# Optimization experiments

Measured on AMD Instinct MI355X. Metric: run time of the kernel, lower is better.

Reference implementation:

```python
import jax, jax.numpy as jnp
import numpy as np

EMB = 768
HEADS = 12
HEAD_DIM = EMB // HEADS
SEQ = 4096
BATCH = 1


def setup_inputs() -> dict:
    key = jax.random.key(0)
    ks = jax.random.split(key, 9)
    s = 1.0 / np.sqrt(EMB)
    return {
        "x": jax.random.normal(ks[0], (BATCH, SEQ, EMB), dtype=jnp.float32),
        "wq": jax.random.normal(ks[1], (EMB, EMB), dtype=jnp.float32) * s,
        "bq": jax.random.normal(ks[2], (EMB,), dtype=jnp.float32) * s,
        "wk": jax.random.normal(ks[3], (EMB, EMB), dtype=jnp.float32) * s,
        "bk": jax.random.normal(ks[4], (EMB,), dtype=jnp.float32) * s,
        "wv": jax.random.normal(ks[5], (EMB, EMB), dtype=jnp.float32) * s,
        "bv": jax.random.normal(ks[6], (EMB,), dtype=jnp.float32) * s,
        "wo": jax.random.normal(ks[7], (EMB, EMB), dtype=jnp.float32) * s,
        "bo": jax.random.normal(ks[8], (EMB,), dtype=jnp.float32) * s,
    }


def reference(x, wq, bq, wk, bk, wv, bv, wo, bo):
    b, n, _ = x.shape
    # projections: [b, n, emb] -> [b, heads, n, head_dim]
    def split_heads(t):
        return t.reshape(b, n, HEADS, HEAD_DIM).transpose(0, 2, 1, 3)
    q = split_heads(x @ wq + bq)
    k = split_heads(x @ wk + bk)
    v = split_heads(x @ wv + bv)
    # full N x N scores (naive attention, as in the original)
    scores = jnp.einsum("bhqd,bhkd->bhqk", q, k)
    causal = jnp.triu(jnp.ones((n, n), dtype=bool), k=1)
    scores = jnp.where(causal, -jnp.inf, scores)
    weights = jax.nn.softmax(scores / np.sqrt(HEAD_DIM), axis=-1)
    # dropout with rate 0.0 is identity (eval mode)
    ctx = jnp.einsum("bhqk,bhkd->bhqd", weights, v)
    ctx = ctx.transpose(0, 2, 1, 3).reshape(b, n, EMB)
    return ctx @ wo + bo
```

## Files before the change

kernel.cpp:

```cpp
#include <hip/hip_runtime.h>
#include <stdint.h>

#define SEQ 4096
#define EMB 768
#define HEADS 12
#define HD 64
#define NQT (SEQ / 64)

typedef __attribute__((ext_vector_type(8))) short short8;
typedef __attribute__((ext_vector_type(4))) short short4v;
typedef __attribute__((ext_vector_type(8))) __bf16 bf16x8;
typedef __attribute__((ext_vector_type(4))) __bf16 bf16x4;
typedef __attribute__((ext_vector_type(4))) float f32x4;

#define QSCALE 0.18033688011112043f

static __device__ __forceinline__ unsigned short f2bf(float f) {
    unsigned int u = __builtin_bit_cast(unsigned int, f);
    unsigned int r = 0x7fffu + ((u >> 16) & 1u);
    u += r;
    return (unsigned short)(u >> 16);
}

static __device__ __forceinline__ f32x4 mfma32(short8 a, short8 b, f32x4 c) {
    return __builtin_amdgcn_mfma_f32_16x16x32_bf16(
        __builtin_bit_cast(bf16x8, a), __builtin_bit_cast(bf16x8, b), c, 0, 0, 0);
}

static __device__ __forceinline__ f32x4 mfma16(short4v a, short4v b, f32x4 c) {
#if __has_builtin(__builtin_amdgcn_mfma_f32_16x16x16_bf16)
    return __builtin_amdgcn_mfma_f32_16x16x16_bf16(
        __builtin_bit_cast(bf16x4, a), __builtin_bit_cast(bf16x4, b), c, 0, 0, 0);
#else
    return __builtin_amdgcn_mfma_f32_16x16x16bf16_1k(a, b, c, 0, 0, 0);
#endif
}

static __device__ __forceinline__ short4v pack4bf(float a, float b, float c, float d) {
#if __has_builtin(__builtin_amdgcn_cvt_pk_bf16_f32)
    typedef __attribute__((ext_vector_type(2))) __bf16 bf16x2;
    bf16x2 lo = __builtin_amdgcn_cvt_pk_bf16_f32(a, b);
    bf16x2 hi = __builtin_amdgcn_cvt_pk_bf16_f32(c, d);
    uint2 u = {__builtin_bit_cast(unsigned int, lo), __builtin_bit_cast(unsigned int, hi)};
    return __builtin_bit_cast(short4v, u);
#else
    short4v p;
    p[0] = (short)f2bf(a); p[1] = (short)f2bf(b);
    p[2] = (short)f2bf(c); p[3] = (short)f2bf(d);
    return p;
#endif
}

static __device__ __forceinline__ void load_lds16(const void* g, void* l) {
    __builtin_amdgcn_global_load_lds(
        (const __attribute__((address_space(1))) unsigned int*)(uintptr_t)g,
        (__attribute__((address_space(3))) unsigned int*)(uintptr_t)l, 16, 0, 0);
}

__global__ __launch_bounds__(256) void convert_x(const float* __restrict__ x,
                                                 unsigned short* __restrict__ xb) {
    int i = blockIdx.x * 256 + threadIdx.x;
    float4 v = ((const float4*)x)[i];
    ushort4 o = {f2bf(v.x), f2bf(v.y), f2bf(v.z), f2bf(v.w)};
    ((ushort4*)xb)[i] = o;
}

__global__ __launch_bounds__(256) void convert_w(const float* __restrict__ wq,
                                                 const float* __restrict__ wk,
                                                 const float* __restrict__ wv,
                                                 const float* __restrict__ wo,
                                                 unsigned short* __restrict__ wqkvT,
                                                 unsigned short* __restrict__ woT) {
    __shared__ unsigned short Ls[64][72];
    const int z = blockIdx.z;
    const float* W = (z == 0) ? wq : (z == 1) ? wk : (z == 2) ? wv : wo;
    unsigned short* dst = (z < 3) ? (wqkvT + (size_t)z * EMB * EMB) : woT;
    const int k0 = blockIdx.x * 64, n0 = blockIdx.y * 64;
    const int r = threadIdx.x >> 2, c0 = (threadIdx.x & 3) * 16;
    for (int j = 0; j < 16; j += 4) {
        float4 v = *(const float4*)&W[(size_t)(k0 + r) * EMB + n0 + c0 + j];
        Ls[r][c0 + j] = f2bf(v.x);
        Ls[r][c0 + j + 1] = f2bf(v.y);
        Ls[r][c0 + j + 2] = f2bf(v.z);
        Ls[r][c0 + j + 3] = f2bf(v.w);
    }
    __syncthreads();
    unsigned short tmp[16];
    for (int j = 0; j < 16; j++) tmp[j] = Ls[c0 + j][r];
    *(uint4*)&dst[(size_t)(n0 + r) * EMB + k0 + c0] = *(uint4*)tmp;
    *(uint4*)&dst[(size_t)(n0 + r) * EMB + k0 + c0 + 8] = *(uint4*)(tmp + 8);
}

template <int MODE>
__global__ __launch_bounds__(256) void gemm128(const unsigned short* __restrict__ A,
                                               const unsigned short* __restrict__ Bt,
                                               const float* __restrict__ b0p,
                                               const float* __restrict__ b1p,
                                               const float* __restrict__ b2p,
                                               unsigned short* __restrict__ Qb,
                                               unsigned short* __restrict__ Kb,
                                               unsigned short* __restrict__ Vtb,
                                               float* __restrict__ outp) {
    __shared__ __align__(16) unsigned short As[128 * 32];
    __shared__ __align__(16) unsigned short Bs[128 * 32];
    const int tid = threadIdx.x;
    const int wave = tid >> 6, lane = tid & 63, quad = lane >> 4, l16 = lane & 15;
    const int m0 = blockIdx.x * 128, n0 = blockIdx.y * 128;
    const int wm = (wave >> 1) * 64, wn = (wave & 1) * 64;
    const int lrow = lane >> 2, lcol = (lane & 3) * 8;

    f32x4 acc[4][4] = {};

    for (int k0 = 0; k0 < EMB; k0 += 32) {
        __syncthreads();
        for (int t = 0; t < 2; t++) {
            int row = wave * 32 + t * 16 + lrow;
            load_lds16(&A[(size_t)(m0 + row) * EMB + k0 + lcol], &As[(wave * 2 + t) * 512]);
            load_lds16(&Bt[(size_t)(n0 + row) * EMB + k0 + lcol], &Bs[(wave * 2 + t) * 512]);
        }
        __syncthreads();
        short8 a[4], b[4];
        for (int i = 0; i < 4; i++) a[i] = *(const short8*)&As[(wm + i * 16 + l16) * 32 + quad * 8];
        for (int i = 0; i < 4; i++) b[i] = *(const short8*)&Bs[(wn + i * 16 + l16) * 32 + quad * 8];
        for (int i = 0; i < 4; i++)
            for (int j = 0; j < 4; j++) acc[i][j] = mfma32(a[i], b[j], acc[i][j]);
    }

    if (MODE == 1) {
        for (int i = 0; i < 4; i++)
            for (int j = 0; j < 4; j++) {
                int mbase = m0 + wm + i * 16 + quad * 4;
                int n = n0 + wn + j * 16 + l16;
                float bv = b0p[n];
                for (int r = 0; r < 4; r++) outp[(size_t)(mbase + r) * EMB + n] = acc[i][j][r] + bv;
            }
    } else {
        const int z = n0 / EMB;
        const float* bias = (z == 0) ? b0p : (z == 1) ? b1p : b2p;
        for (int i = 0; i < 4; i++)
            for (int j = 0; j < 4; j++) {
                int mbase = m0 + wm + i * 16 + quad * 4;
                int n = n0 + wn + j * 16 + l16;
                int nn = n - z * EMB;
                int h = nn >> 6, d = nn & 63;
                float bv = bias[nn];
                if (z == 0) {
                    for (int r = 0; r < 4; r++)
                        Qb[(size_t)(h * SEQ + mbase + r) * HD + d] =
                            f2bf((acc[i][j][r] + bv) * QSCALE);
                } else if (z == 1) {
                    for (int r = 0; r < 4; r++)
                        Kb[(size_t)(h * SEQ + mbase + r) * HD + d] = f2bf(acc[i][j][r] + bv);
                } else {
                    ushort4 pk;
                    pk.x = f2bf(acc[i][j][0] + bv);
                    pk.y = f2bf(acc[i][j][1] + bv);
                    pk.z = f2bf(acc[i][j][2] + bv);
                    pk.w = f2bf(acc[i][j][3] + bv);
                    *(ushort4*)&Vtb[(size_t)(h * HD + d) * SEQ + mbase] = pk;
                }
            }
    }
}

__global__ __launch_bounds__(256) void attn_kernel(const unsigned short* __restrict__ Qb,
                                                   const unsigned short* __restrict__ Kb,
                                                   const unsigned short* __restrict__ Vtb,
                                                   unsigned short* __restrict__ ctxb) {
    __shared__ __align__(16) unsigned short Qs[64 * 72];
    __shared__ __align__(16) unsigned short Ks[64 * 72];
    __shared__ __align__(16) unsigned short Vs[64 * 72];

    const int bid = blockIdx.x;
    const int h = bid % HEADS;
    const int qt = (NQT - 1) - bid / HEADS;
    const int qbase = qt * 64;
    const int tid = threadIdx.x;
    const int wave = tid >> 6, lane = tid & 63, quad = lane >> 4, l16 = lane & 15;

    const unsigned short* Qh = Qb + (size_t)h * SEQ * HD;
    const unsigned short* Kh = Kb + (size_t)h * SEQ * HD;
    const unsigned short* Vh = Vtb + (size_t)h * HD * SEQ;

    const int row = tid >> 2, cg = (tid & 3) * 16;
    *(uint4*)&Qs[row * 72 + cg] = *(const uint4*)&Qh[(size_t)(qbase + row) * HD + cg];
    *(uint4*)&Qs[row * 72 + cg + 8] = *(const uint4*)&Qh[(size_t)(qbase + row) * HD + cg + 8];
    __syncthreads();
    const short8 bQ0 = *(const short8*)&Qs[(wave * 16 + l16) * 72 + quad * 8];
    const short8 bQ1 = *(const short8*)&Qs[(wave * 16 + l16) * 72 + 32 + quad * 8];
    const int q = qbase + wave * 16 + l16;

    f32x4 O[4] = {};
    float m_i = -3.0e38f, l_i = 0.f;

    uint4 kr0, kr1, vr0, vr1;
    {
        kr0 = *(const uint4*)&Kh[(size_t)row * HD + cg];
        kr1 = *(const uint4*)&Kh[(size_t)row * HD + cg + 8];
        vr0 = *(const uint4*)&Vh[(size_t)row * SEQ + cg];
        vr1 = *(const uint4*)&Vh[(size_t)row * SEQ + cg + 8];
    }

    for (int kt = 0; kt <= qt; kt++) {
        const int kbase = kt * 64;
        __syncthreads();
        *(uint4*)&Ks[row * 72 + cg] = kr0;
        *(uint4*)&Ks[row * 72 + cg + 8] = kr1;
        *(uint4*)&Vs[row * 72 + cg] = vr0;
        *(uint4*)&Vs[row * 72 + cg + 8] = vr1;
        if (kt < qt) {
            const int nb = kbase + 64;
            kr0 = *(const uint4*)&Kh[(size_t)(nb + row) * HD + cg];
            kr1 = *(const uint4*)&Kh[(size_t)(nb + row) * HD + cg + 8];
            vr0 = *(const uint4*)&Vh[(size_t)row * SEQ + nb + cg];
            vr1 = *(const uint4*)&Vh[(size_t)row * SEQ + nb + cg + 8];
        }
        __syncthreads();

        f32x4 st[4];
        for (int nt = 0; nt < 4; nt++) {
            short8 aK0 = *(const short8*)&Ks[(nt * 16 + l16) * 72 + quad * 8];
            short8 aK1 = *(const short8*)&Ks[(nt * 16 + l16) * 72 + 32 + quad * 8];
            f32x4 z = {};
            z = mfma32(aK0, bQ0, z);
            z = mfma32(aK1, bQ1, z);
            st[nt] = z;
        }
        if (kt == qt) {
            for (int nt = 0; nt < 4; nt++)
                for (int r = 0; r < 4; r++)
                    if (kbase + nt * 16 + quad * 4 + r > q) st[nt][r] = -INFINITY;
        }
        float mx = -3.0e38f;
        for (int nt = 0; nt < 4; nt++)
            for (int r = 0; r < 4; r++) mx = fmaxf(mx, st[nt][r]);
        mx = fmaxf(mx, __shfl_xor(mx, 16));
        mx = fmaxf(mx, __shfl_xor(mx, 32));
        const float mn = fmaxf(m_i, mx);
        const float alpha = __builtin_amdgcn_exp2f(m_i - mn);
        m_i = mn;
        float rs = 0.f;
        short4v pk[4];
        for (int nt = 0; nt < 4; nt++) {
            float p0 = __builtin_amdgcn_exp2f(st[nt][0] - mn);
            float p1 = __builtin_amdgcn_exp2f(st[nt][1] - mn);
            float p2 = __builtin_amdgcn_exp2f(st[nt][2] - mn);
            float p3 = __builtin_amdgcn_exp2f(st[nt][3] - mn);
            rs += p0 + p1 + p2 + p3;
            pk[nt] = pack4bf(p0, p1, p2, p3);
        }
        rs += __shfl_xor(rs, 16);
        rs += __shfl_xor(rs, 32);
        l_i = l_i * alpha + rs;
        for (int dt = 0; dt < 4; dt++)
            for (int r = 0; r < 4; r++) O[dt][r] *= alpha;
        for (int dt = 0; dt < 4; dt++)
            for (int nt = 0; nt < 4; nt++) {
                short4v av = *(const short4v*)&Vs[(dt * 16 + l16) * 72 + nt * 16 + quad * 4];
                O[dt] = mfma16(av, pk[nt], O[dt]);
            }
    }

    const float inv = 1.f / l_i;
    for (int dt = 0; dt < 4; dt++) {
        ushort4 o;
        o.x = f2bf(O[dt][0] * inv);
        o.y = f2bf(O[dt][1] * inv);
        o.z = f2bf(O[dt][2] * inv);
        o.w = f2bf(O[dt][3] * inv);
        *(ushort4*)&ctxb[(size_t)q * EMB + h * HD + dt * 16 + quad * 4] = o;
    }
}

extern "C" void kernel_launch(void* const* d_in, const int* in_sizes, int n_in,
                              void* d_out, int out_size, void* d_ws, size_t ws_size,
                              hipStream_t stream) {
    const float* x = (const float*)d_in[0];
    const float* wq = (const float*)d_in[1];
    const float* bq = (const float*)d_in[2];
    const float* wk = (const float*)d_in[3];
    const float* bk = (const float*)d_in[4];
    const float* wv = (const float*)d_in[5];
    const float* bv = (const float*)d_in[6];
    const float* wo = (const float*)d_in[7];
    const float* bo = (const float*)d_in[8];

    unsigned short* ws = (unsigned short*)d_ws;
    unsigned short* xb = ws;
    unsigned short* wqkvT = xb + SEQ * EMB;
    unsigned short* woT = wqkvT + 3 * EMB * EMB;
    unsigned short* Qb = woT + EMB * EMB;
    unsigned short* Kb = Qb + HEADS * SEQ * HD;
    unsigned short* Vtb = Kb + HEADS * SEQ * HD;
    unsigned short* ctxb = Vtb + HEADS * SEQ * HD;

    convert_x<<<dim3(SEQ * EMB / 4 / 256), 256, 0, stream>>>(x, xb);
    convert_w<<<dim3(12, 12, 4), 256, 0, stream>>>(wq, wk, wv, wo, wqkvT, woT);
    gemm128<0><<<dim3(SEQ / 128, 3 * EMB / 128), 256, 0, stream>>>(
        xb, wqkvT, bq, bk, bv, Qb, Kb, Vtb, nullptr);
    attn_kernel<<<dim3(NQT * HEADS), 256, 0, stream>>>(Qb, Kb, Vtb, ctxb);
    gemm128<1><<<dim3(SEQ / 128, EMB / 128), 256, 0, stream>>>(
        ctxb, woT, bo, nullptr, nullptr, nullptr, nullptr, nullptr, (float*)d_out);
}
```

Before: 218.9 us.

## Split long causal attention rows across two blocks and merge partial softmax results

Query tiles in the upper half of the sequence are split along the key dimension into two blocks, each writing unnormalized partial outputs plus running max and sum. A new merge kernel combines them. This balances the causal work per block and adds blocks for better occupancy. The change also stores Q and K in a combined row-major [seq, 1536] layout, skips the rescale when no lane's max grows (wave ballot), and transposes fp32 before converting in convert_w. It costs an extra kernel launch, bf16 rounding of the partial outputs, and reuse of workspace regions for the partials.

```diff
diff --git a/kernel.cpp b/kernel.cpp
--- a/kernel.cpp
+++ b/kernel.cpp
@@ -71,7 +71,7 @@
                                                  const float* __restrict__ wo,
                                                  unsigned short* __restrict__ wqkvT,
                                                  unsigned short* __restrict__ woT) {
-    __shared__ unsigned short Ls[64][72];
+    __shared__ float Ls[64][65];
     const int z = blockIdx.z;
     const float* W = (z == 0) ? wq : (z == 1) ? wk : (z == 2) ? wv : wo;
     unsigned short* dst = (z < 3) ? (wqkvT + (size_t)z * EMB * EMB) : woT;
@@ -79,14 +79,14 @@
     const int r = threadIdx.x >> 2, c0 = (threadIdx.x & 3) * 16;
     for (int j = 0; j < 16; j += 4) {
         float4 v = *(const float4*)&W[(size_t)(k0 + r) * EMB + n0 + c0 + j];
-        Ls[r][c0 + j] = f2bf(v.x);
-        Ls[r][c0 + j + 1] = f2bf(v.y);
-        Ls[r][c0 + j + 2] = f2bf(v.z);
-        Ls[r][c0 + j + 3] = f2bf(v.w);
+        Ls[r][c0 + j] = v.x;
+        Ls[r][c0 + j + 1] = v.y;
+        Ls[r][c0 + j + 2] = v.z;
+        Ls[r][c0 + j + 3] = v.w;
     }
     __syncthreads();
     unsigned short tmp[16];
-    for (int j = 0; j < 16; j++) tmp[j] = Ls[c0 + j][r];
+    for (int j = 0; j < 16; j++) tmp[j] = f2bf(Ls[c0 + j][r]);
     *(uint4*)&dst[(size_t)(n0 + r) * EMB + k0 + c0] = *(uint4*)tmp;
     *(uint4*)&dst[(size_t)(n0 + r) * EMB + k0 + c0 + 8] = *(uint4*)(tmp + 8);
 }
@@ -97,8 +97,7 @@
                                                const float* __restrict__ b0p,
                                                const float* __restrict__ b1p,
                                                const float* __restrict__ b2p,
-                                               unsigned short* __restrict__ Qb,
-                                               unsigned short* __restrict__ Kb,
+                                               unsigned short* __restrict__ QKb,
                                                unsigned short* __restrict__ Vtb,
                                                float* __restrict__ outp) {
     __shared__ __align__(16) unsigned short As[128 * 32];
@@ -136,22 +135,24 @@
             }
     } else {
         const int z = n0 / EMB;
-        const float* bias = (z == 0) ? b0p : (z == 1) ? b1p : b2p;
-        for (int i = 0; i < 4; i++)
-            for (int j = 0; j < 4; j++) {
-                int mbase = m0 + wm + i * 16 + quad * 4;
-                int n = n0 + wn + j * 16 + l16;
-                int nn = n - z * EMB;
-                int h = nn >> 6, d = nn & 63;
-                float bv = bias[nn];
-                if (z == 0) {
+        if (z < 2) {
+            const float* bias = z ? b1p : b0p;
+            const float sc = z ? 1.0f : QSCALE;
+            for (int i = 0; i < 4; i++)
+                for (int j = 0; j < 4; j++) {
+                    int mbase = m0 + wm + i * 16 + quad * 4;
+                    int n = n0 + wn + j * 16 + l16;
+                    float bv = bias[n - z * EMB];
                     for (int r = 0; r < 4; r++)
-                        Qb[(size_t)(h * SEQ + mbase + r) * HD + d] =
-                            f2bf((acc[i][j][r] + bv) * QSCALE);
-                } else if (z == 1) {
-                    for (int r = 0; r < 4; r++)
-                        Kb[(size_t)(h * SEQ + mbase + r) * HD + d] = f2bf(acc[i][j][r] + bv);
-                } else {
+                        QKb[(size_t)(mbase + r) * 1536 + n] = f2bf((acc[i][j][r] + bv) * sc);
+                }
+        } else {
+            for (int i = 0; i < 4; i++)
+                for (int j = 0; j < 4; j++) {
+                    int mbase = m0 + wm + i * 16 + quad * 4;
+                    int nn = n0 + wn + j * 16 + l16 - 2 * EMB;
+                    int h = nn >> 6, d = nn & 63;
+                    float bv = b2p[nn];
                     ushort4 pk;
                     pk.x = f2bf(acc[i][j][0] + bv);
                     pk.y = f2bf(acc[i][j][1] + bv);
@@ -159,32 +160,49 @@
                     pk.w = f2bf(acc[i][j][3] + bv);
                     *(ushort4*)&Vtb[(size_t)(h * HD + d) * SEQ + mbase] = pk;
                 }
-            }
-    }
-}
-
-__global__ __launch_bounds__(256) void attn_kernel(const unsigned short* __restrict__ Qb,
-                                                   const unsigned short* __restrict__ Kb,
+        }
+    }
+}
+
+__global__ __launch_bounds__(256) void attn_kernel(const unsigned short* __restrict__ QKb,
                                                    const unsigned short* __restrict__ Vtb,
-                                                   unsigned short* __restrict__ ctxb) {
+                                                   unsigned short* __restrict__ ctxb,
+                                                   unsigned short* __restrict__ Op,
+                                                   float* __restrict__ mArr,
+                                                   float* __restrict__ lArr) {
     __shared__ __align__(16) unsigned short Qs[64 * 72];
     __shared__ __align__(16) unsigned short Ks[64 * 72];
     __shared__ __align__(16) unsigned short Vs[64 * 72];
 
     const int bid = blockIdx.x;
-    const int h = bid % HEADS;
-    const int qt = (NQT - 1) - bid / HEADS;
+    int s, h, qt, kb, ke;
+    if (bid < 768) {
+        s = bid & 1;
+        int idx = bid >> 1;
+        qt = 63 - idx / 12;
+        h = idx % 12;
+        int h0 = (qt + 2) >> 1;
+        kb = s ? h0 : 0;
+        ke = s ? qt : h0 - 1;
+    } else {
+        s = -1;
+        int idx = bid - 768;
+        qt = 31 - idx / 12;
+        h = idx % 12;
+        kb = 0;
+        ke = qt;
+    }
     const int qbase = qt * 64;
     const int tid = threadIdx.x;
     const int wave = tid >> 6, lane = tid & 63, quad = lane >> 4, l16 = lane & 15;
 
-    const unsigned short* Qh = Qb + (size_t)h * SEQ * HD;
-    const unsigned short* Kh = Kb + (size_t)h * SEQ * HD;
+    const unsigned short* Qg = QKb + (size_t)h * HD;
+    const unsigned short* Kg = QKb + (size_t)(EMB + h * HD);
     const unsigned short* Vh = Vtb + (size_t)h * HD * SEQ;
 
     const int row = tid >> 2, cg = (tid & 3) * 16;
-    *(uint4*)&Qs[row * 72 + cg] = *(const uint4*)&Qh[(size_t)(qbase + row) * HD + cg];
-    *(uint4*)&Qs[row * 72 + cg + 8] = *(const uint4*)&Qh[(size_t)(qbase + row) * HD + cg + 8];
+    *(uint4*)&Qs[row * 72 + cg] = *(const uint4*)&Qg[(size_t)(qbase + row) * 1536 + cg];
+    *(uint4*)&Qs[row * 72 + cg + 8] = *(const uint4*)&Qg[(size_t)(qbase + row) * 1536 + cg + 8];
     __syncthreads();
     const short8 bQ0 = *(const short8*)&Qs[(wave * 16 + l16) * 72 + quad * 8];
     const short8 bQ1 = *(const short8*)&Qs[(wave * 16 + l16) * 72 + 32 + quad * 8];
@@ -195,23 +213,24 @@
 
     uint4 kr0, kr1, vr0, vr1;
     {
-        kr0 = *(const uint4*)&Kh[(size_t)row * HD + cg];
-        kr1 = *(const uint4*)&Kh[(size_t)row * HD + cg + 8];
-        vr0 = *(const uint4*)&Vh[(size_t)row * SEQ + cg];
-        vr1 = *(const uint4*)&Vh[(size_t)row * SEQ + cg + 8];
-    }
-
-    for (int kt = 0; kt <= qt; kt++) {
+        const int kb64 = kb * 64;
+        kr0 = *(const uint4*)&Kg[(size_t)(kb64 + row) * 1536 + cg];
+        kr1 = *(const uint4*)&Kg[(size_t)(kb64 + row) * 1536 + cg + 8];
+        vr0 = *(const uint4*)&Vh[(size_t)row * SEQ + kb64 + cg];
+        vr1 = *(const uint4*)&Vh[(size_t)row * SEQ + kb64 + cg + 8];
+    }
+
+    for (int kt = kb; kt <= ke; kt++) {
         const int kbase = kt * 64;
         __syncthreads();
         *(uint4*)&Ks[row * 72 + cg] = kr0;
         *(uint4*)&Ks[row * 72 + cg + 8] = kr1;
         *(uint4*)&Vs[row * 72 + cg] = vr0;
         *(uint4*)&Vs[row * 72 + cg + 8] = vr1;
-        if (kt < qt) {
+        if (kt < ke) {
             const int nb = kbase + 64;
-            kr0 = *(const uint4*)&Kh[(size_t)(nb + row) * HD + cg];
-            kr1 = *(const uint4*)&Kh[(size_t)(nb + row) * HD + cg + 8];
+            kr0 = *(const uint4*)&Kg[(size_t)(nb + row) * 1536 + cg];
+            kr1 = *(const uint4*)&Kg[(size_t)(nb + row) * 1536 + cg + 8];
             vr0 = *(const uint4*)&Vh[(size_t)row * SEQ + nb + cg];
             vr1 = *(const uint4*)&Vh[(size_t)row * SEQ + nb + cg + 8];
         }
@@ -236,24 +255,28 @@
             for (int r = 0; r < 4; r++) mx = fmaxf(mx, st[nt][r]);
         mx = fmaxf(mx, __shfl_xor(mx, 16));
         mx = fmaxf(mx, __shfl_xor(mx, 32));
-        const float mn = fmaxf(m_i, mx);
-        const float alpha = __builtin_amdgcn_exp2f(m_i - mn);
-        m_i = mn;
+        const bool inc = mx > m_i;
+        if (__ballot(inc)) {
+            const float mn = inc ? mx : m_i;
+            const float alpha = __builtin_amdgcn_exp2f(m_i - mn);
+            m_i = mn;
+            l_i *= alpha;
+            for (int dt = 0; dt < 4; dt++)
+                for (int r = 0; r < 4; r++) O[dt][r] *= alpha;
+        }
         float rs = 0.f;
         short4v pk[4];
         for (int nt = 0; nt < 4; nt++) {
-            float p0 = __builtin_amdgcn_exp2f(st[nt][0] - mn);
-            float p1 = __builtin_amdgcn_exp2f(st[nt][1] - mn);
-            float p2 = __builtin_amdgcn_exp2f(st[nt][2] - mn);
-            float p3 = __builtin_amdgcn_exp2f(st[nt][3] - mn);
+            float p0 = __builtin_amdgcn_exp2f(st[nt][0] - m_i);
+            float p1 = __builtin_amdgcn_exp2f(st[nt][1] - m_i);
+            float p2 = __builtin_amdgcn_exp2f(st[nt][2] - m_i);
+            float p3 = __builtin_amdgcn_exp2f(st[nt][3] - m_i);
             rs += p0 + p1 + p2 + p3;
             pk[nt] = pack4bf(p0, p1, p2, p3);
         }
         rs += __shfl_xor(rs, 16);
         rs += __shfl_xor(rs, 32);
-        l_i = l_i * alpha + rs;
-        for (int dt = 0; dt < 4; dt++)
-            for (int r = 0; r < 4; r++) O[dt][r] *= alpha;
+        l_i += rs;
         for (int dt = 0; dt < 4; dt++)
             for (int nt = 0; nt < 4; nt++) {
                 short4v av = *(const short4v*)&Vs[(dt * 16 + l16) * 72 + nt * 16 + quad * 4];
@@ -261,14 +284,64 @@
             }
     }
 
-    const float inv = 1.f / l_i;
-    for (int dt = 0; dt < 4; dt++) {
-        ushort4 o;
-        o.x = f2bf(O[dt][0] * inv);
-        o.y = f2bf(O[dt][1] * inv);
-        o.z = f2bf(O[dt][2] * inv);
-        o.w = f2bf(O[dt][3] * inv);
-        *(ushort4*)&ctxb[(size_t)q * EMB + h * HD + dt * 16 + quad * 4] = o;
+    const int ql = wave * 16 + l16;
+    if (s < 0) {
+        const float inv = 1.f / l_i;
+        for (int dt = 0; dt < 4; dt++) {
+            ushort4 o;
+            o.x = f2bf(O[dt][0] * inv);
+            o.y = f2bf(O[dt][1] * inv);
+            o.z = f2bf(O[dt][2] * inv);
+            o.w = f2bf(O[dt][3] * inv);
+            *(ushort4*)&ctxb[(size_t)q * EMB + h * HD + dt * 16 + quad * 4] = o;
+        }
+    } else {
+        const int pb = (s * HEADS + h) * 32 + (qt - 32);
+        for (int dt = 0; dt < 4; dt++) {
+            ushort4 o;
+            o.x = f2bf(O[dt][0]);
+            o.y = f2bf(O[dt][1]);
+            o.z = f2bf(O[dt][2]);
+            o.w = f2bf(O[dt][3]);
+            *(ushort4*)&Op[(size_t)pb * 4096 + ql * 64 + dt * 16 + quad * 4] = o;
+        }
+        if (quad == 0) {
+            mArr[pb * 64 + ql] = m_i;
+            lArr[pb * 64 + ql] = l_i;
+        }
+    }
+}
+
+__global__ __launch_bounds__(256) void merge_kernel(const unsigned short* __restrict__ Op,
+                                                    const float* __restrict__ mArr,
+                                                    const float* __restrict__ lArr,
+                                                    unsigned short* __restrict__ ctxb) {
+    const int idx = blockIdx.x;
+    const int qt = 32 + idx / HEADS;
+    const int h = idx % HEADS;
+    const int q = threadIdx.x >> 2, d0 = (threadIdx.x & 3) * 16;
+    const int pb0 = h * 32 + (qt - 32);
+    const int pb1 = (HEADS + h) * 32 + (qt - 32);
+    const float m0 = mArr[pb0 * 64 + q], m1 = mArr[pb1 * 64 + q];
+    const float l0 = lArr[pb0 * 64 + q], l1 = lArr[pb1 * 64 + q];
+    const float M = fmaxf(m0, m1);
+    float a0 = __builtin_amdgcn_exp2f(m0 - M);
+    float a1 = __builtin_amdgcn_exp2f(m1 - M);
+    const float inv = 1.f / (a0 * l0 + a1 * l1);
+    a0 *= inv;
+    a1 *= inv;
+    for (int jj = 0; jj < 16; jj += 8) {
+        uint4 u0 = *(const uint4*)&Op[(size_t)pb0 * 4096 + q * 64 + d0 + jj];
+        uint4 u1 = *(const uint4*)&Op[(size_t)pb1 * 4096 + q * 64 + d0 + jj];
+        const unsigned short* p0 = (const unsigned short*)&u0;
+        const unsigned short* p1 = (const unsigned short*)&u1;
+        unsigned short o[8];
+        for (int t = 0; t < 8; t++) {
+            float f0 = __builtin_bit_cast(float, (unsigned int)p0[t] << 16);
+            float f1 = __builtin_bit_cast(float, (unsigned int)p1[t] << 16);
+            o[t] = f2bf(a0 * f0 + a1 * f1);
+        }
+        *(uint4*)&ctxb[(size_t)(qt * 64 + q) * EMB + h * HD + d0 + jj] = *(uint4*)o;
     }
 }
 
@@ -289,16 +362,19 @@
     unsigned short* xb = ws;
     unsigned short* wqkvT = xb + SEQ * EMB;
     unsigned short* woT = wqkvT + 3 * EMB * EMB;
-    unsigned short* Qb = woT + EMB * EMB;
-    unsigned short* Kb = Qb + HEADS * SEQ * HD;
-    unsigned short* Vtb = Kb + HEADS * SEQ * HD;
+    unsigned short* QKb = woT + EMB * EMB;
+    unsigned short* Vtb = QKb + (size_t)SEQ * 1536;
     unsigned short* ctxb = Vtb + HEADS * SEQ * HD;
+    unsigned short* Op = xb;
+    float* mArr = (float*)wqkvT;
+    float* lArr = mArr + 768 * 64;
 
     convert_x<<<dim3(SEQ * EMB / 4 / 256), 256, 0, stream>>>(x, xb);
     convert_w<<<dim3(12, 12, 4), 256, 0, stream>>>(wq, wk, wv, wo, wqkvT, woT);
     gemm128<0><<<dim3(SEQ / 128, 3 * EMB / 128), 256, 0, stream>>>(
-        xb, wqkvT, bq, bk, bv, Qb, Kb, Vtb, nullptr);
-    attn_kernel<<<dim3(NQT * HEADS), 256, 0, stream>>>(Qb, Kb, Vtb, ctxb);
+        xb, wqkvT, bq, bk, bv, QKb, Vtb, nullptr);
+    attn_kernel<<<dim3(1152), 256, 0, stream>>>(QKb, Vtb, ctxb, Op, mArr, lArr);
+    merge_kernel<<<dim3(384), 256, 0, stream>>>(Op, mArr, lArr, ctxb);
     gemm128<1><<<dim3(SEQ / 128, EMB / 128), 256, 0, stream>>>(
-        ctxb, woT, bo, nullptr, nullptr, nullptr, nullptr, nullptr, (float*)d_out);
-}
+        ctxb, woT, bo, nullptr, nullptr, nullptr, nullptr, (float*)d_out);
+}
```

Measured after the change: 209.2 us. 1.05x faster.
